# Optimization experiments

Hardware: AMD Instinct MI355X
Metric: run time of the kernel (lower is better)

The kernel has to match this reference:

```python
import jax, jax.numpy as jnp
import numpy as np

S = 7
NB = 2          # boxes per cell
C = 20          # classes
L_COORD = 5.0
L_NOOBJ = 0.5
IMG = 448.0
GRID = 64.0
BATCH = 8192


def _make_ground_truth(key):
    k1, k2, k3, k4 = jax.random.split(key, 4)
    xy = jax.random.uniform(k1, (BATCH, S, S, 2), jnp.float32, 0.05, 0.95)
    wh = jax.random.uniform(k2, (BATCH, S, S, 2), jnp.float32, 0.05, 0.8)
    obj = (jax.random.uniform(k3, (BATCH, S, S)) < 0.15).astype(jnp.float32)
    cls = jax.nn.one_hot(jax.random.randint(k4, (BATCH, S, S), 0, C), C, dtype=jnp.float32)
    gridX = jnp.arange(S, dtype=jnp.float32)[None, None, :]  # column index
    gridY = jnp.arange(S, dtype=jnp.float32)[None, :, None]  # row index
    cx = (xy[..., 0] + gridX) * GRID
    cy = (xy[..., 1] + gridY) * GRID
    w = wh[..., 0] * IMG
    h = wh[..., 1] * IMG
    x1 = jnp.maximum(0.0, cx - w / 2)
    y1 = jnp.maximum(0.0, cy - h / 2)
    x2 = jnp.minimum(IMG - 1.0, cx + w / 2)
    y2 = jnp.minimum(IMG - 1.0, cy + h / 2)
    area = (x2 - x1) * (y2 - y1)
    return jnp.concatenate(
        [xy, wh, obj[..., None], x1[..., None], y1[..., None],
         x2[..., None], y2[..., None], area[..., None], cls], axis=-1)


def setup_inputs() -> dict:
    key = jax.random.key(0)
    k1, k2 = jax.random.split(key)
    # predictions in (0,1) so sqrt() in the coord loss is well defined
    bounding_boxes = jax.random.uniform(k1, (BATCH, S, S, NB * 5 + C),
                                        jnp.float32, 1e-3, 1.0)
    ground_truth = _make_ground_truth(k2)
    return {"bounding_boxes": bounding_boxes, "ground_truth": ground_truth}


def _iou(box, gt):
    # box: [B,S,S,5]; gt: [B,S,S,30]. Mirrors the original int() truncation.
    gridX = jnp.arange(S, dtype=box.dtype)[None, None, :]
    gridY = jnp.arange(S, dtype=box.dtype)[None, :, None]
    px = jnp.trunc((box[..., 0] + gridX) * GRID)
    py = jnp.trunc((box[..., 1] + gridY) * GRID)
    pw = jnp.trunc(box[..., 2] * IMG)
    ph = jnp.trunc(box[..., 3] * IMG)
    x1 = jnp.maximum(0.0, px - pw / 2)
    y1 = jnp.maximum(0.0, py - ph / 2)
    x2 = jnp.minimum(IMG - 1.0, px + pw / 2)
    y2 = jnp.minimum(IMG - 1.0, py + ph / 2)
    parea = (x2 - x1) * (y2 - y1)
    lx = jnp.maximum(x1, gt[..., 5])
    rx = jnp.minimum(x2, gt[..., 7])
    uy = jnp.maximum(y1, gt[..., 6])
    dy = jnp.minimum(y2, gt[..., 8])
    inter = (rx - lx) * (dy - uy)
    valid = (rx >= lx) & (dy >= uy)
    return jnp.where(valid, inter / (parea + gt[..., 9] - inter), 0.0)


def reference(bounding_boxes, ground_truth):
    gt = ground_truth
    b1 = bounding_boxes[..., 0:5]
    b2 = bounding_boxes[..., 5:10]
    # IoU computed via numpy/.item() in torch -> detached from autograd
    iou1 = jax.lax.stop_gradient(_iou(b1, gt))
    iou2 = jax.lax.stop_gradient(_iou(b2, gt))
    resp1 = iou1 > iou2  # tie -> box two, matching the original strict '>'
    pbox = jnp.where(resp1[..., None], b1, b2)
    nbox = jnp.where(resp1[..., None], b2, b1)
    iou = jnp.where(resp1, iou1, iou2)

    mask = jnp.round(gt[..., 4]) != 0
    fm = mask.astype(bounding_boxes.dtype)

    noobj = L_NOOBJ * (b1[..., 4] ** 2 + b2[..., 4] ** 2)
    coord = L_COORD * ((pbox[..., 0] - gt[..., 0]) ** 2
                       + (pbox[..., 1] - gt[..., 1]) ** 2
                       + (jnp.sqrt(pbox[..., 2]) - jnp.sqrt(gt[..., 2])) ** 2
                       + (jnp.sqrt(pbox[..., 3]) - jnp.sqrt(gt[..., 3])) ** 2)
    conf = (pbox[..., 4] - iou) ** 2 + L_NOOBJ * nbox[..., 4] ** 2
    cls_loss = jnp.sum((gt[..., 10:] - bounding_boxes[..., NB * 5:]) ** 2, axis=-1)

    loss = jnp.sum(fm * (coord + conf + cls_loss) + (1.0 - fm) * noobj)
    loss_coord = jnp.sum(fm * coord)
    loss_confidence = jnp.sum(fm * conf + (1.0 - fm) * noobj)
    loss_classes = jnp.sum(fm * cls_loss)
    iou_sum = jnp.sum(fm * iou)
    object_num = jnp.sum(mask.astype(jnp.int32))
    return (loss, loss_coord, loss_confidence, loss_classes, iou_sum, object_num)
```

## Files before the change

### kernel.cpp

```cpp
#include <hip/hip_runtime.h>


#define CH 30
#define NCELLS (8192 * 49)
#define NPAIRS (NCELLS / 2)
#define BLK 256
#define NBLOCKS (NPAIRS / BLK)

__device__ __forceinline__ float iou_one(const float* __restrict__ B,
                                         const float* __restrict__ G,
                                         float fx, float fy) {
    float px = truncf((B[0] + fx) * 64.0f);
    float py = truncf((B[1] + fy) * 64.0f);
    float pw = truncf(B[2] * 448.0f);
    float ph = truncf(B[3] * 448.0f);
    float x1 = fmaxf(0.0f, px - pw * 0.5f);
    float y1 = fmaxf(0.0f, py - ph * 0.5f);
    float x2 = fminf(447.0f, px + pw * 0.5f);
    float y2 = fminf(447.0f, py + ph * 0.5f);
    float parea = (x2 - x1) * (y2 - y1);
    float lx = fmaxf(x1, G[5]);
    float rx = fminf(x2, G[7]);
    float uy = fmaxf(y1, G[6]);
    float dy = fminf(y2, G[8]);
    float inter = (rx - lx) * (dy - uy);
    bool valid = (rx >= lx) && (dy >= uy);
    return valid ? inter / (parea + G[9] - inter) : 0.0f;
}

__global__ __launch_bounds__(256) void yolo_v1_loss_main(
    const float* __restrict__ bb, const float* __restrict__ gt,
    float* __restrict__ ws) {
    __shared__ float sRed[4][6];

    const int tid = threadIdx.x;
    const int pair = blockIdx.x * BLK + tid;

    const float4* pb = (const float4*)bb + (size_t)pair * 15;
    const float4* pg = (const float4*)gt + (size_t)pair * 15;

    float vb[60], vg[60];
#pragma unroll
    for (int i = 0; i < 15; ++i) {
        *(float4*)(vb + 4 * i) = pb[i];
        *(float4*)(vg + 4 * i) = pg[i];
    }

    float a_loss = 0.f, a_coord = 0.f, a_conf = 0.f, a_cls = 0.f,
          a_iou = 0.f, a_obj = 0.f;

#pragma unroll
    for (int c = 0; c < 2; ++c) {
        const float* B = vb + 30 * c;
        const float* G = vg + 30 * c;

        int cell = pair * 2 + c;
        int b = cell / 49;
        int rem = cell - b * 49;
        int gy = rem / 7;
        int gx = rem - gy * 7;
        float fx = (float)gx, fy = (float)gy;

        float iou1 = iou_one(B, G, fx, fy);
        float iou2 = iou_one(B + 5, G, fx, fy);
        bool r1 = iou1 > iou2;
        const float* P = r1 ? B : (B + 5);
        const float* Nb = r1 ? (B + 5) : B;
        float iou = r1 ? iou1 : iou2;

        float fm = (rintf(G[4]) != 0.0f) ? 1.0f : 0.0f;

        float noobj = 0.5f * (B[4] * B[4] + B[9] * B[9]);

        float dx = P[0] - G[0];
        float dyv = P[1] - G[1];
        float dw = sqrtf(P[2]) - sqrtf(G[2]);
        float dh = sqrtf(P[3]) - sqrtf(G[3]);
        float coord = 5.0f * (dx * dx + dyv * dyv + dw * dw + dh * dh);

        float dc = P[4] - iou;
        float conf = dc * dc + 0.5f * Nb[4] * Nb[4];

        float cls = 0.f;
#pragma unroll
        for (int k = 0; k < 20; ++k) {
            float d = G[10 + k] - B[10 + k];
            cls += d * d;
        }

        float ifm = 1.0f - fm;
        a_loss += fm * (coord + conf + cls) + ifm * noobj;
        a_coord += fm * coord;
        a_conf += fm * conf + ifm * noobj;
        a_cls += fm * cls;
        a_iou += fm * iou;
        a_obj += fm;
    }

#pragma unroll
    for (int off = 32; off > 0; off >>= 1) {
        a_loss += __shfl_down(a_loss, off);
        a_coord += __shfl_down(a_coord, off);
        a_conf += __shfl_down(a_conf, off);
        a_cls += __shfl_down(a_cls, off);
        a_iou += __shfl_down(a_iou, off);
        a_obj += __shfl_down(a_obj, off);
    }
    int wave = tid >> 6;
    int lane = tid & 63;
    if (lane == 0) {
        sRed[wave][0] = a_loss;
        sRed[wave][1] = a_coord;
        sRed[wave][2] = a_conf;
        sRed[wave][3] = a_cls;
        sRed[wave][4] = a_iou;
        sRed[wave][5] = a_obj;
    }
    __syncthreads();
    if (tid == 0) {
#pragma unroll
        for (int j = 0; j < 6; ++j) {
            float v = sRed[0][j] + sRed[1][j] + sRed[2][j] + sRed[3][j];
            ws[j * NBLOCKS + blockIdx.x] = v;
        }
    }
}

__global__ __launch_bounds__(384) void yolo_v1_loss_reduce(
    const float* __restrict__ ws, float* __restrict__ out) {
    const int tid = threadIdx.x;
    const int j = tid >> 6;
    const int lane = tid & 63;
    float s = 0.f;
    for (int i = lane; i < NBLOCKS; i += 64) s += ws[j * NBLOCKS + i];
#pragma unroll
    for (int off = 32; off > 0; off >>= 1) s += __shfl_down(s, off);
    if (lane == 0) out[j] = s;
}

extern "C" void kernel_launch(void* const* d_in, const int* in_sizes, int n_in,
                              void* d_out, int out_size, void* d_ws,
                              size_t ws_size, hipStream_t stream) {
    const float* bb = (const float*)d_in[0];
    const float* gt = (const float*)d_in[1];
    float* out = (float*)d_out;
    float* ws = (float*)d_ws;
    yolo_v1_loss_main<<<NBLOCKS, BLK, 0, stream>>>(bb, gt, ws);
    yolo_v1_loss_reduce<<<1, 384, 0, stream>>>(ws, out);
}
```

Measured before the change: 27.60 us.

## Stage cell tiles into LDS with async global_load_lds and prefetch next tile

Each wavefront now processes contiguous 64-cell tiles, copying bounding-box and ground-truth data into LDS with global_load_lds. Each load covers a fully coalesced 1 KiB span, replacing per-thread strided float4 loads. The second tile is prefetched while the first is computed, and the per-block LDS/syncthreads reduction is replaced by per-wave partial writes into the workspace. The aim is to improve memory coalescing and overlap loads with compute. The cost is manual waitcnt management and more LDS per block, which may limit occupancy.

```diff
diff --git a/kernel.cpp b/kernel.cpp
--- a/kernel.cpp
+++ b/kernel.cpp
@@ -3,9 +3,13 @@
 
 #define CH 30
 #define NCELLS (8192 * 49)
-#define NPAIRS (NCELLS / 2)
+#define TCELLS 64
+#define TBYTES (TCELLS * CH * 4)
+#define NTILES (NCELLS / TCELLS)
 #define BLK 256
-#define NBLOCKS (NPAIRS / BLK)
+#define WPB (BLK / 64)
+#define GRID_BLOCKS 784
+#define NW (GRID_BLOCKS * WPB)
 
 __device__ __forceinline__ float iou_one(const float* __restrict__ B,
                                          const float* __restrict__ G,
@@ -28,38 +32,72 @@
     return valid ? inter / (parea + G[9] - inter) : 0.0f;
 }
 
+__device__ __forceinline__ void stage_tile(const char* __restrict__ bb,
+                                           const char* __restrict__ gt,
+                                           char* lbase, int tile, int lane) {
+    const char* bbt = bb + (size_t)tile * TBYTES;
+    const char* gtt = gt + (size_t)tile * TBYTES;
+#pragma unroll
+    for (int i = 0; i < 15; ++i) {
+        int f = i * 1024 + lane * 16;
+        const char* src = (f < TBYTES) ? (bbt + f) : (gtt + (f - TBYTES));
+        __builtin_amdgcn_global_load_lds(
+            (const __attribute__((address_space(1))) void*)src,
+            (__attribute__((address_space(3))) void*)(lbase + i * 1024), 16, 0,
+            0);
+    }
+}
+
 __global__ __launch_bounds__(256) void yolo_v1_loss_main(
-    const float* __restrict__ bb, const float* __restrict__ gt,
+    const float* __restrict__ bbf, const float* __restrict__ gtf,
     float* __restrict__ ws) {
-    __shared__ float sRed[4][6];
+    __shared__ char lds[WPB][2 * TBYTES];
 
     const int tid = threadIdx.x;
-    const int pair = blockIdx.x * BLK + tid;
+    const int lane = tid & 63;
+    const int w = tid >> 6;
+    const int gw = blockIdx.x * WPB + w;
 
-    const float4* pb = (const float4*)bb + (size_t)pair * 15;
-    const float4* pg = (const float4*)gt + (size_t)pair * 15;
-
-    float vb[60], vg[60];
-#pragma unroll
-    for (int i = 0; i < 15; ++i) {
-        *(float4*)(vb + 4 * i) = pb[i];
-        *(float4*)(vg + 4 * i) = pg[i];
-    }
+    const char* bb = (const char*)bbf;
+    const char* gt = (const char*)gtf;
+    char* lbase = lds[w];
 
     float a_loss = 0.f, a_coord = 0.f, a_conf = 0.f, a_cls = 0.f,
           a_iou = 0.f, a_obj = 0.f;
 
+    stage_tile(bb, gt, lbase, gw, lane);
+
 #pragma unroll
-    for (int c = 0; c < 2; ++c) {
-        const float* B = vb + 30 * c;
-        const float* G = vg + 30 * c;
+    for (int it = 0; it < 2; ++it) {
+        const int tile = gw + it * NW;
 
-        int cell = pair * 2 + c;
+        asm volatile("s_waitcnt vmcnt(0)" ::: "memory");
+        __builtin_amdgcn_sched_barrier(0);
+
+        float vb[CH], vg[CH];
+        const float2* pb2 = (const float2*)(lbase + lane * (CH * 4));
+        const float2* pg2 = (const float2*)(lbase + TBYTES + lane * (CH * 4));
+#pragma unroll
+        for (int i = 0; i < 15; ++i) {
+            *(float2*)(vb + 2 * i) = pb2[i];
+            *(float2*)(vg + 2 * i) = pg2[i];
+        }
+
+        if (it == 0) {
+            asm volatile("s_waitcnt lgkmcnt(0)" ::: "memory");
+            __builtin_amdgcn_sched_barrier(0);
+            stage_tile(bb, gt, lbase, gw + NW, lane);
+        }
+
+        int cell = tile * TCELLS + lane;
         int b = cell / 49;
         int rem = cell - b * 49;
         int gy = rem / 7;
         int gx = rem - gy * 7;
         float fx = (float)gx, fy = (float)gy;
+
+        const float* B = vb;
+        const float* G = vg;
 
         float iou1 = iou_one(B, G, fx, fy);
         float iou2 = iou_one(B + 5, G, fx, fy);
@@ -69,7 +107,6 @@
         float iou = r1 ? iou1 : iou2;
 
         float fm = (rintf(G[4]) != 0.0f) ? 1.0f : 0.0f;
-
         float noobj = 0.5f * (B[4] * B[4] + B[9] * B[9]);
 
         float dx = P[0] - G[0];
@@ -106,23 +143,13 @@
         a_iou += __shfl_down(a_iou, off);
         a_obj += __shfl_down(a_obj, off);
     }
-    int wave = tid >> 6;
-    int lane = tid & 63;
     if (lane == 0) {
-        sRed[wave][0] = a_loss;
-        sRed[wave][1] = a_coord;
-        sRed[wave][2] = a_conf;
-        sRed[wave][3] = a_cls;
-        sRed[wave][4] = a_iou;
-        sRed[wave][5] = a_obj;
-    }
-    __syncthreads();
-    if (tid == 0) {
-#pragma unroll
-        for (int j = 0; j < 6; ++j) {
-            float v = sRed[0][j] + sRed[1][j] + sRed[2][j] + sRed[3][j];
-            ws[j * NBLOCKS + blockIdx.x] = v;
-        }
+        ws[0 * NW + gw] = a_loss;
+        ws[1 * NW + gw] = a_coord;
+        ws[2 * NW + gw] = a_conf;
+        ws[3 * NW + gw] = a_cls;
+        ws[4 * NW + gw] = a_iou;
+        ws[5 * NW + gw] = a_obj;
     }
 }
 
@@ -132,7 +159,7 @@
     const int j = tid >> 6;
     const int lane = tid & 63;
     float s = 0.f;
-    for (int i = lane; i < NBLOCKS; i += 64) s += ws[j * NBLOCKS + i];
+    for (int i = lane; i < NW; i += 64) s += ws[j * NW + i];
 #pragma unroll
     for (int off = 32; off > 0; off >>= 1) s += __shfl_down(s, off);
     if (lane == 0) out[j] = s;
@@ -145,6 +172,6 @@
     const float* gt = (const float*)d_in[1];
     float* out = (float*)d_out;
     float* ws = (float*)d_ws;
-    yolo_v1_loss_main<<<NBLOCKS, BLK, 0, stream>>>(bb, gt, ws);
+    yolo_v1_loss_main<<<GRID_BLOCKS, BLK, 0, stream>>>(bb, gt, ws);
     yolo_v1_loss_reduce<<<1, 384, 0, stream>>>(ws, out);
 }
```

Result: slower. 37.82 us (+37.0%).

## Process one cell per thread with split even/odd grid halves

Applied to the files above, without the earlier changes.

Each thread now handles a single cell instead of a pair. The first half of the grid takes even cells and the second half takes odd cells, each loading an aligned 8-float4 window (128 B) that covers its 30 floats. The goal is to halve register pressure (32+32 floats instead of 60+60), raise occupancy via launch_bounds(256,5), and double the block count for latency hiding. The cost is that every thread loads 2 extra float4s of overlapping data, about 7% more traffic, and the second-stage reduction has twice as many partials, now reduced with 768 threads.

```diff
diff --git a/kernel.cpp b/kernel.cpp
--- a/kernel.cpp
+++ b/kernel.cpp
@@ -3,9 +3,9 @@
 
 #define CH 30
 #define NCELLS (8192 * 49)
-#define NPAIRS (NCELLS / 2)
 #define BLK 256
-#define NBLOCKS (NPAIRS / BLK)
+#define NBLK (NCELLS / BLK)
+#define HBLK (NBLK / 2)
 
 __device__ __forceinline__ float iou_one(const float* __restrict__ B,
                                          const float* __restrict__ G,
@@ -28,114 +28,114 @@
     return valid ? inter / (parea + G[9] - inter) : 0.0f;
 }
 
-__global__ __launch_bounds__(256) void yolo_v1_loss_main(
-    const float* __restrict__ bb, const float* __restrict__ gt,
+template <int OFF>
+__device__ __forceinline__ void do_cell(const float4* __restrict__ b4,
+                                        const float4* __restrict__ g4,
+                                        size_t f4idx, int cell, float acc[6]) {
+    float vb[32], vg[32];
+#pragma unroll
+    for (int i = 0; i < 8; ++i) {
+        *(float4*)(vb + 4 * i) = b4[f4idx + i];
+        *(float4*)(vg + 4 * i) = g4[f4idx + i];
+    }
+    const float* B = vb + OFF;
+    const float* G = vg + OFF;
+
+    int rem = cell % 49;
+    int gy = rem / 7;
+    int gx = rem - gy * 7;
+    float fx = (float)gx, fy = (float)gy;
+
+    float iou1 = iou_one(B, G, fx, fy);
+    float iou2 = iou_one(B + 5, G, fx, fy);
+    bool r1 = iou1 > iou2;
+    const float* P = r1 ? B : (B + 5);
+    const float* Nb = r1 ? (B + 5) : B;
+    float iou = r1 ? iou1 : iou2;
+
+    float fm = (rintf(G[4]) != 0.0f) ? 1.0f : 0.0f;
+    float noobj = 0.5f * (B[4] * B[4] + B[9] * B[9]);
+
+    float dx = P[0] - G[0];
+    float dyv = P[1] - G[1];
+    float dw = sqrtf(P[2]) - sqrtf(G[2]);
+    float dh = sqrtf(P[3]) - sqrtf(G[3]);
+    float coord = 5.0f * (dx * dx + dyv * dyv + dw * dw + dh * dh);
+
+    float dc = P[4] - iou;
+    float conf = dc * dc + 0.5f * Nb[4] * Nb[4];
+
+    float cls = 0.f;
+#pragma unroll
+    for (int k = 0; k < 20; ++k) {
+        float d = G[10 + k] - B[10 + k];
+        cls += d * d;
+    }
+
+    float ifm = 1.0f - fm;
+    acc[0] += fm * (coord + conf + cls) + ifm * noobj;
+    acc[1] += fm * coord;
+    acc[2] += fm * conf + ifm * noobj;
+    acc[3] += fm * cls;
+    acc[4] += fm * iou;
+    acc[5] += fm;
+}
+
+__global__ __launch_bounds__(256, 5) void yolo_v1_loss_main(
+    const float* __restrict__ bbf, const float* __restrict__ gtf,
     float* __restrict__ ws) {
     __shared__ float sRed[4][6];
 
     const int tid = threadIdx.x;
-    const int pair = blockIdx.x * BLK + tid;
+    const int bid = blockIdx.x;
+    const float4* b4 = (const float4*)bbf;
+    const float4* g4 = (const float4*)gtf;
 
-    const float4* pb = (const float4*)bb + (size_t)pair * 15;
-    const float4* pg = (const float4*)gt + (size_t)pair * 15;
+    float acc[6] = {0.f, 0.f, 0.f, 0.f, 0.f, 0.f};
 
-    float vb[60], vg[60];
-#pragma unroll
-    for (int i = 0; i < 15; ++i) {
-        *(float4*)(vb + 4 * i) = pb[i];
-        *(float4*)(vg + 4 * i) = pg[i];
-    }
-
-    float a_loss = 0.f, a_coord = 0.f, a_conf = 0.f, a_cls = 0.f,
-          a_iou = 0.f, a_obj = 0.f;
-
-#pragma unroll
-    for (int c = 0; c < 2; ++c) {
-        const float* B = vb + 30 * c;
-        const float* G = vg + 30 * c;
-
-        int cell = pair * 2 + c;
-        int b = cell / 49;
-        int rem = cell - b * 49;
-        int gy = rem / 7;
-        int gx = rem - gy * 7;
-        float fx = (float)gx, fy = (float)gy;
-
-        float iou1 = iou_one(B, G, fx, fy);
-        float iou2 = iou_one(B + 5, G, fx, fy);
-        bool r1 = iou1 > iou2;
-        const float* P = r1 ? B : (B + 5);
-        const float* Nb = r1 ? (B + 5) : B;
-        float iou = r1 ? iou1 : iou2;
-
-        float fm = (rintf(G[4]) != 0.0f) ? 1.0f : 0.0f;
-
-        float noobj = 0.5f * (B[4] * B[4] + B[9] * B[9]);
-
-        float dx = P[0] - G[0];
-        float dyv = P[1] - G[1];
-        float dw = sqrtf(P[2]) - sqrtf(G[2]);
-        float dh = sqrtf(P[3]) - sqrtf(G[3]);
-        float coord = 5.0f * (dx * dx + dyv * dyv + dw * dw + dh * dh);
-
-        float dc = P[4] - iou;
-        float conf = dc * dc + 0.5f * Nb[4] * Nb[4];
-
-        float cls = 0.f;
-#pragma unroll
-        for (int k = 0; k < 20; ++k) {
-            float d = G[10 + k] - B[10 + k];
-            cls += d * d;
-        }
-
-        float ifm = 1.0f - fm;
-        a_loss += fm * (coord + conf + cls) + ifm * noobj;
-        a_coord += fm * coord;
-        a_conf += fm * conf + ifm * noobj;
-        a_cls += fm * cls;
-        a_iou += fm * iou;
-        a_obj += fm;
+    if (bid < HBLK) {
+        size_t u = (size_t)bid * BLK + tid;
+        do_cell<0>(b4, g4, 15 * u, (int)(2 * u), acc);
+    } else {
+        size_t u = (size_t)(bid - HBLK) * BLK + tid;
+        do_cell<2>(b4, g4, 15 * u + 7, (int)(2 * u + 1), acc);
     }
 
 #pragma unroll
     for (int off = 32; off > 0; off >>= 1) {
-        a_loss += __shfl_down(a_loss, off);
-        a_coord += __shfl_down(a_coord, off);
-        a_conf += __shfl_down(a_conf, off);
-        a_cls += __shfl_down(a_cls, off);
-        a_iou += __shfl_down(a_iou, off);
-        a_obj += __shfl_down(a_obj, off);
+#pragma unroll
+        for (int j = 0; j < 6; ++j) acc[j] += __shfl_down(acc[j], off);
     }
     int wave = tid >> 6;
     int lane = tid & 63;
     if (lane == 0) {
-        sRed[wave][0] = a_loss;
-        sRed[wave][1] = a_coord;
-        sRed[wave][2] = a_conf;
-        sRed[wave][3] = a_cls;
-        sRed[wave][4] = a_iou;
-        sRed[wave][5] = a_obj;
+#pragma unroll
+        for (int j = 0; j < 6; ++j) sRed[wave][j] = acc[j];
     }
     __syncthreads();
     if (tid == 0) {
 #pragma unroll
         for (int j = 0; j < 6; ++j) {
-            float v = sRed[0][j] + sRed[1][j] + sRed[2][j] + sRed[3][j];
-            ws[j * NBLOCKS + blockIdx.x] = v;
+            ws[j * NBLK + bid] =
+                sRed[0][j] + sRed[1][j] + sRed[2][j] + sRed[3][j];
         }
     }
 }
 
-__global__ __launch_bounds__(384) void yolo_v1_loss_reduce(
+__global__ __launch_bounds__(768) void yolo_v1_loss_reduce(
     const float* __restrict__ ws, float* __restrict__ out) {
+    __shared__ float sp[12];
     const int tid = threadIdx.x;
-    const int j = tid >> 6;
-    const int lane = tid & 63;
+    const int j = tid >> 7;
+    const int sub = tid & 127;
     float s = 0.f;
-    for (int i = lane; i < NBLOCKS; i += 64) s += ws[j * NBLOCKS + i];
+    for (int i = sub; i < NBLK; i += 128) s += ws[j * NBLK + i];
 #pragma unroll
     for (int off = 32; off > 0; off >>= 1) s += __shfl_down(s, off);
-    if (lane == 0) out[j] = s;
+    const int wave = tid >> 6;
+    if ((tid & 63) == 0) sp[wave] = s;
+    __syncthreads();
+    if (tid < 6) out[tid] = sp[2 * tid] + sp[2 * tid + 1];
 }
 
 extern "C" void kernel_launch(void* const* d_in, const int* in_sizes, int n_in,
@@ -145,6 +145,6 @@
     const float* gt = (const float*)d_in[1];
     float* out = (float*)d_out;
     float* ws = (float*)d_ws;
-    yolo_v1_loss_main<<<NBLOCKS, BLK, 0, stream>>>(bb, gt, ws);
-    yolo_v1_loss_reduce<<<1, 384, 0, stream>>>(ws, out);
+    yolo_v1_loss_main<<<NBLK, BLK, 0, stream>>>(bb, gt, ws);
+    yolo_v1_loss_reduce<<<1, 768, 0, stream>>>(ws, out);
 }
```

Result: slower. 43.72 us (+58.4%).
